# Kernel tuning notes

Hardware: AMD Instinct MI355X
Metric: run time of the kernel (lower is better)

The kernel has to match this reference:

```python
import jax, jax.numpy as jnp
import numpy as np

B, S, H, NH = 2, 2048, 4096, 32
D = H // NH  # head_dim = 128


def setup_inputs() -> dict:
    key = jax.random.key(0)
    ks = jax.random.split(key, 9)
    s = 1.0 / np.sqrt(H)
    return {
        "hidden_state": jax.random.normal(ks[0], (B, S, H), jnp.float32),
        "Wq": jax.random.normal(ks[1], (H, H), jnp.float32) * s,
        "bq": jax.random.normal(ks[2], (H,), jnp.float32) * 0.01,
        "Wk": jax.random.normal(ks[3], (D, H), jnp.float32) * s,
        "bk": jax.random.normal(ks[4], (D,), jnp.float32) * 0.01,
        "Wv": jax.random.normal(ks[5], (D, H), jnp.float32) * s,
        "bv": jax.random.normal(ks[6], (D,), jnp.float32) * 0.01,
        "Wo": jax.random.normal(ks[7], (H, H), jnp.float32) * s,
        "bo": jax.random.normal(ks[8], (H,), jnp.float32) * 0.01,
    }


def reference(hidden_state, Wq, bq, Wk, bk, Wv, bv, Wo, bo):
    b = hidden_state.shape[0]
    # Projections (torch Linear: x @ W.T + b)
    q = hidden_state @ Wq.T + bq              # (b, s, H)
    k = hidden_state @ Wk.T + bk              # (b, s, D) single shared KV head
    v = hidden_state @ Wv.T + bv              # (b, s, D)
    q = q.reshape(b, -1, NH, D).transpose(0, 2, 1, 3)  # (b, nh, s, d)
    # scores: broadcast the single K head across all query heads
    scale = 1.0 / jnp.sqrt(jnp.float32(D))
    scores = jnp.einsum("bhqd,bkd->bhqk", q, k) * scale   # (b, nh, s, s)
    probs = jax.nn.softmax(scores, axis=-1)
    out = jnp.einsum("bhqk,bkd->bhqd", probs, v)           # (b, nh, s, d)
    # Faithful to source: transpose(-1,-2) then view(b, -1, nh*d)
    out = jnp.swapaxes(out, -1, -2).reshape(b, -1, NH * D)  # (b, s, H) scrambled layout
    return out @ Wo.T + bo
```

## Files before the change

### kernel.cpp

```cpp
#include <hip/hip_runtime.h>
#include <hip/hip_bf16.h>

typedef __attribute__((ext_vector_type(8))) short bf16x8;
typedef __attribute__((ext_vector_type(4))) float f32x4;
typedef __attribute__((ext_vector_type(4))) unsigned int u32x4;
typedef __attribute__((ext_vector_type(2))) unsigned int u32x2;

__device__ __forceinline__ unsigned short f2bf(float f) {
    unsigned u = __builtin_bit_cast(unsigned, f);
    u += 0x7FFFu + ((u >> 16) & 1u);
    return (unsigned short)(u >> 16);
}

__device__ __forceinline__ void async16(const void* g, void* l) {
    __builtin_amdgcn_global_load_lds(
        (const __attribute__((address_space(1))) unsigned int*)g,
        (__attribute__((address_space(3))) unsigned int*)l, 16, 0, 0);
}

template <int N> __device__ __forceinline__ void waitv() {
    if constexpr (N == 8)      asm volatile("s_waitcnt vmcnt(8)" ::: "memory");
    else if constexpr (N == 6) asm volatile("s_waitcnt vmcnt(6)" ::: "memory");
    else if constexpr (N == 4) asm volatile("s_waitcnt vmcnt(4)" ::: "memory");
    else if constexpr (N == 3) asm volatile("s_waitcnt vmcnt(3)" ::: "memory");
    else                       asm volatile("s_waitcnt vmcnt(0)" ::: "memory");
}
#define BARF() do { __builtin_amdgcn_s_barrier(); asm volatile("" ::: "memory"); } while (0)

__device__ __forceinline__ void pl32(unsigned &a, unsigned &b) {
    u32x2 r = __builtin_amdgcn_permlane32_swap(a, b, false, false);
    a = r[0]; b = r[1];
}
__device__ __forceinline__ void pl16(unsigned &a, unsigned &b) {
    u32x2 r = __builtin_amdgcn_permlane16_swap(a, b, false, false);
    a = r[0]; b = r[1];
}

__global__ void cvt_f32_bf16(const float* __restrict__ x, unsigned short* __restrict__ y, int n4) {
    const int stride = gridDim.x * blockDim.x;
    for (int i = blockIdx.x * blockDim.x + threadIdx.x; i < n4; i += stride) {
        const float4 v = ((const float4*)x)[i];
        ushort4 o;
        o.x = f2bf(v.x); o.y = f2bf(v.y); o.z = f2bf(v.z); o.w = f2bf(v.w);
        ((ushort4*)y)[i] = o;
    }
}

template <int MREP, int MODE>
__global__ __launch_bounds__(512, 2) void gemm256(
    const unsigned short* __restrict__ A, const unsigned short* __restrict__ Bt,
    const float* __restrict__ b0, const float* __restrict__ b1, const float* __restrict__ b2,
    void* __restrict__ o0, unsigned short* __restrict__ o1, unsigned short* __restrict__ o2)
{
    constexpr int K = 4096, NT = 128;
    constexpr int ACALLS = MREP / 4;
    constexpr int CALLS  = ACALLS + 2;
    constexpr int ASH    = MREP * 1024;
    constexpr int SLOT   = ASH + 8192;
    __shared__ __align__(16) unsigned short lds[4 * SLOT];

    const int tid  = threadIdx.x;
    const int w    = tid >> 6, lane = tid & 63;
    const int l16  = lane & 15, quad = lane >> 4;
    const int wm   = w >> 2, wn = w & 3;

    int bx, by;
    {
        const int wg = (int)blockIdx.x;
        if constexpr (MODE == 1) {
            const int wgp = (wg & 7) * 68 + (wg >> 3);
            bx = wgp / 32; by = wgp % 32;
        } else {
            const int wgp = (wg & 7) * 32 + (wg >> 3);
            bx = wgp / 16; by = wgp % 16;
        }
    }
    const int m0 = by * (MREP * 32);
    const int n0 = bx * 256;

    const int srow = lane >> 2;
    const int schk = ((lane & 3) ^ ((lane >> 3) & 3)) * 8;
    const unsigned short* gAs[ACALLS];
#pragma unroll
    for (int c = 0; c < ACALLS; ++c)
        gAs[c] = A + (size_t)(m0 + (w * ACALLS + c) * 16 + srow) * K + schk;
    const unsigned short* gBs[2];
#pragma unroll
    for (int c = 0; c < 2; ++c)
        gBs[c] = Bt + (size_t)(n0 + (w * 2 + c) * 16 + srow) * K + schk;

    const int swz8 = (quad ^ ((l16 >> 1) & 3)) * 8;
    const int aoff = (wm * (MREP * 16) + l16) * 32 + swz8;
    const int boff = ASH + (wn * 64 + l16) * 32 + swz8;

    f32x4 acc[MREP][4] = {};

#define STAGE(tt) do { \
    unsigned short* lb = &lds[((tt) & 3) * SLOT]; \
    _Pragma("unroll") \
    for (int c = 0; c < ACALLS; ++c) \
        async16(gAs[c] + (tt) * 32, lb + (w * ACALLS + c) * 512); \
    _Pragma("unroll") \
    for (int c = 0; c < 2; ++c) \
        async16(gBs[c] + (tt) * 32, lb + ASH + (w * 2 + c) * 512); \
} while (0)

#define BODY(tt) do { \
    const unsigned short* lb = &lds[((tt) & 3) * SLOT]; \
    bf16x8 af[MREP], bfr[4]; \
    _Pragma("unroll") \
    for (int i = 0; i < MREP; ++i) af[i] = *(const bf16x8*)(lb + aoff + i * 512); \
    _Pragma("unroll") \
    for (int j = 0; j < 4; ++j)    bfr[j] = *(const bf16x8*)(lb + boff + j * 512); \
    __builtin_amdgcn_s_setprio(1); \
    _Pragma("unroll") \
    for (int i = 0; i < MREP; ++i) { \
        _Pragma("unroll") \
        for (int j = 0; j < 4; ++j) \
            acc[i][j] = __builtin_amdgcn_mfma_f32_16x16x32_bf16(af[i], bfr[j], acc[i][j], 0, 0, 0); \
    } \
    __builtin_amdgcn_s_setprio(0); \
} while (0)

    STAGE(0); STAGE(1); STAGE(2);
    for (int t = 0; t < NT - 3; ++t) {
        waitv<CALLS * 2>();
        BARF();
        STAGE(t + 3);
        BODY(t);
    }
    waitv<CALLS * 2>(); BARF(); BODY(NT - 3);
    waitv<CALLS>();     BARF(); BODY(NT - 2);
    waitv<0>();         BARF(); BODY(NT - 1);

#undef STAGE
#undef BODY

    if constexpr (MODE == 0) {
        float* C = (float*)o0;
#pragma unroll
        for (int j = 0; j < 4; ++j) {
            const int n = n0 + wn * 64 + j * 16 + l16;
            const float bb = b0[n];
#pragma unroll
            for (int i = 0; i < MREP; ++i) {
                const int mb = m0 + wm * (MREP * 16) + i * 16 + quad * 4;
#pragma unroll
                for (int r = 0; r < 4; ++r)
                    C[(size_t)(mb + r) * 4096 + n] = acc[i][j][r] + bb;
            }
        }
    } else {
        unsigned short* q_out = (unsigned short*)o0;
        const int nw0 = n0 + wn * 64;
        if (nw0 < 4096) {
#pragma unroll
            for (int j = 0; j < 4; ++j) {
                const int n = nw0 + j * 16 + l16;
                const float bb = b0[n];
#pragma unroll
                for (int i = 0; i < MREP; ++i) {
                    const int mb = m0 + wm * (MREP * 16) + i * 16 + quad * 4;
#pragma unroll
                    for (int r = 0; r < 4; ++r)
                        q_out[(size_t)(mb + r) * 4096 + n] = f2bf(acc[i][j][r] + bb);
                }
            }
        } else if (nw0 < 4224) {
#pragma unroll
            for (int j = 0; j < 4; ++j) {
                const int d = nw0 - 4096 + j * 16 + l16;
                const float bb = b1[d];
#pragma unroll
                for (int i = 0; i < MREP; ++i) {
                    const int mb = m0 + wm * (MREP * 16) + i * 16 + quad * 4;
#pragma unroll
                    for (int r = 0; r < 4; ++r)
                        o1[(size_t)(mb + r) * 128 + d] = f2bf(acc[i][j][r] + bb);
                }
            }
        } else {
#pragma unroll
            for (int j = 0; j < 4; ++j) {
                const int d = nw0 - 4224 + j * 16 + l16;
                const float bb = b2[d];
#pragma unroll
                for (int i = 0; i < MREP; ++i) {
                    const int mb = m0 + wm * (MREP * 16) + i * 16 + quad * 4;
                    ushort4 o;
                    o.x = f2bf(acc[i][j][0] + bb);
                    o.y = f2bf(acc[i][j][1] + bb);
                    o.z = f2bf(acc[i][j][2] + bb);
                    o.w = f2bf(acc[i][j][3] + bb);
                    *(ushort4*)(o2 + (size_t)((mb >> 11) * 128 + d) * 2048 + (mb & 2047)) = o;
                }
            }
        }
    }
}

__global__ __launch_bounds__(256, 4) void attn_mqa(
    const unsigned short* __restrict__ Q,
    const unsigned short* __restrict__ Kb,
    const unsigned short* __restrict__ vT,
    unsigned short* __restrict__ scr)
{
    constexpr int S = 2048, D = 128, H = 4096;
    constexpr float CSC = 0.0883883476483184f * 1.4426950408889634f;

    __shared__ __align__(16) unsigned short lds[17536];

    const int tid = threadIdx.x;
    const int w = tid >> 6, lane = tid & 63;
    const int l16 = lane & 15, quad = lane >> 4;
    const int qb = blockIdx.x & 15;
    const int h  = (blockIdx.x >> 4) & 31;
    const int b  = blockIdx.x >> 9;
    const int q0 = qb * 128;

    bf16x8 qf[2][4];
#pragma unroll
    for (int mi = 0; mi < 2; ++mi)
#pragma unroll
        for (int ks = 0; ks < 4; ++ks)
            qf[mi][ks] = *(const bf16x8*)(Q + (size_t)(b * S + q0 + w * 32 + mi * 16 + l16) * H
                                            + h * D + ks * 32 + quad * 8);

    f32x4 Oa[2][8] = {};
    float l_run[2] = {};

    const unsigned short* gK = Kb + (size_t)(b * S + l16) * D + quad * 8;
    const unsigned short* gV = vT + (size_t)(b * 128 + l16) * 2048 + quad * 8;

#define ASTAGE(tt) do { \
    unsigned short* buf = &lds[((tt) & 1) * 8192]; \
    const int kv0s = (tt) * 32; \
    _Pragma("unroll") \
    for (int c2 = 0; c2 < 2; ++c2) { \
        const int c = w * 2 + c2; \
        async16(gK + (size_t)(kv0s + (c >> 2) * 16) * D + (c & 3) * 32, buf + c * 512); \
        async16(gV + (size_t)(c * 16) * 2048 + kv0s, buf + 4096 + c * 512); \
    } \
} while (0)

    ASTAGE(0);
    for (int t = 0; t < 64; ++t) {
        waitv<0>();
        BARF();
        if (t < 63) ASTAGE(t + 1);

        const unsigned short* Kl = &lds[(t & 1) * 8192];
        const unsigned short* Vl = Kl + 4096;

        f32x4 sf[2][2] = {};
#pragma unroll
        for (int ct = 0; ct < 2; ++ct)
#pragma unroll
            for (int ks = 0; ks < 4; ++ks) {
                const bf16x8 kf = *(const bf16x8*)&Kl[(ct * 4 + ks) * 512 + lane * 8];
#pragma unroll
                for (int mi = 0; mi < 2; ++mi)
                    sf[mi][ct] = __builtin_amdgcn_mfma_f32_16x16x32_bf16(kf, qf[mi][ks], sf[mi][ct], 0, 0, 0);
            }

        bf16x8 pa[2];
#pragma unroll
        for (int mi = 0; mi < 2; ++mi) {
            unsigned cw[2][2];
#pragma unroll
            for (int ct = 0; ct < 2; ++ct) {
                const float p0 = exp2f(sf[mi][ct][0] * CSC);
                const float p1 = exp2f(sf[mi][ct][1] * CSC);
                const float p2 = exp2f(sf[mi][ct][2] * CSC);
                const float p3 = exp2f(sf[mi][ct][3] * CSC);
                l_run[mi] += (p0 + p1) + (p2 + p3);
                asm("v_cvt_pk_bf16_f32 %0, %1, %2" : "=v"(cw[ct][0]) : "v"(p0), "v"(p1));
                asm("v_cvt_pk_bf16_f32 %0, %1, %2" : "=v"(cw[ct][1]) : "v"(p2), "v"(p3));
            }
            unsigned c0 = cw[0][0], c1 = cw[0][1];
            unsigned d0 = cw[1][0], d1 = cw[1][1];
            pl32(c0, d0); pl16(c0, d0);
            pl32(c1, d1); pl16(c1, d1);
            u32x4 t4; t4[0] = c0; t4[1] = c1; t4[2] = d0; t4[3] = d1;
            pa[mi] = __builtin_bit_cast(bf16x8, t4);
        }

        __builtin_amdgcn_s_setprio(1);
#pragma unroll
        for (int nt = 0; nt < 8; ++nt) {
            const bf16x8 vf = *(const bf16x8*)&Vl[nt * 512 + lane * 8];
#pragma unroll
            for (int mi = 0; mi < 2; ++mi)
                Oa[mi][nt] = __builtin_amdgcn_mfma_f32_16x16x32_bf16(pa[mi], vf, Oa[mi][nt], 0, 0, 0);
        }
        __builtin_amdgcn_s_setprio(0);
    }
#undef ASTAGE

    float iv[2][4];
#pragma unroll
    for (int mi = 0; mi < 2; ++mi) {
        float l = l_run[mi];
        l += __shfl_xor(l, 16);
        l += __shfl_xor(l, 32);
        const float linv = 1.f / l;
#pragma unroll
        for (int i = 0; i < 4; ++i)
            iv[mi][i] = __shfl(linv, quad * 4 + i);
    }

    __syncthreads();
#pragma unroll
    for (int mi = 0; mi < 2; ++mi)
#pragma unroll
        for (int nt = 0; nt < 8; ++nt)
#pragma unroll
            for (int i = 0; i < 4; ++i)
                lds[(nt * 16 + l16) * 136 + w * 32 + mi * 16 + quad * 4 + i] =
                    f2bf(Oa[mi][nt][i] * iv[mi][i]);
    __syncthreads();

    const int d = tid >> 1, qh = tid & 1;
    unsigned short* op = scr + (size_t)(b * S + h * 64 + (d >> 1)) * H + (d & 1) * 2048 + q0 + qh * 64;
#pragma unroll
    for (int j = 0; j < 8; ++j)
        *(int4*)(op + j * 8) = *(const int4*)&lds[d * 136 + qh * 64 + j * 8];
}

extern "C" void kernel_launch(void* const* d_in, const int* in_sizes, int n_in,
                              void* d_out, int out_size, void* d_ws, size_t ws_size,
                              hipStream_t stream) {
    (void)in_sizes; (void)n_in; (void)out_size; (void)ws_size;
    const float* hidden = (const float*)d_in[0];
    const float* Wq = (const float*)d_in[1];
    const float* bq = (const float*)d_in[2];
    const float* Wk = (const float*)d_in[3];
    const float* bk = (const float*)d_in[4];
    const float* Wv = (const float*)d_in[5];
    const float* bv = (const float*)d_in[6];
    const float* Wo = (const float*)d_in[7];
    const float* bo = (const float*)d_in[8];

    char* ws = (char*)d_ws;
    const size_t MB = 1048576;
    unsigned short* hb   = (unsigned short*)(ws);
    unsigned short* scr  = hb;
    unsigned short* Wcat = (unsigned short*)(ws + 32 * MB);
    unsigned short* Wob  = Wcat;
    unsigned short* q_b  = (unsigned short*)(ws + 68 * MB);
    unsigned short* k_b  = (unsigned short*)(ws + 100 * MB);
    unsigned short* vT   = (unsigned short*)(ws + 101 * MB);

    cvt_f32_bf16<<<1024, 256, 0, stream>>>(hidden, hb, 16777216 / 4);
    cvt_f32_bf16<<<1024, 256, 0, stream>>>(Wq, Wcat, 16777216 / 4);
    cvt_f32_bf16<<<256, 256, 0, stream>>>(Wk, Wcat + 16777216, 524288 / 4);
    cvt_f32_bf16<<<256, 256, 0, stream>>>(Wv, Wcat + 17301504, 524288 / 4);

    gemm256<4, 1><<<dim3(544), 512, 0, stream>>>(hb, Wcat, bq, bk, bv,
                                                 (void*)q_b, k_b, vT);
    cvt_f32_bf16<<<1024, 256, 0, stream>>>(Wo, Wob, 16777216 / 4);
    attn_mqa<<<1024, 256, 0, stream>>>(q_b, k_b, vT, scr);
    gemm256<8, 0><<<dim3(256), 512, 0, stream>>>(scr, Wob, bo, nullptr, nullptr,
                                                 (void*)d_out, nullptr, nullptr);
}
```

Baseline: 725.1 us.

## Fuse input conversions, triple-buffer GEMM for occupancy, fold softmax scale into Q

Merges the four f32-to-bf16 conversion launches into one kernel. The GEMM drops from a 4-slot to a 3-slot LDS ring with rotating offsets and raises launch bounds to 4 blocks per CU. The output projection moves to the smaller MREP=4 tile with 512 blocks and a new block mapping. The softmax scale and log2e factor are folded into the Q projection epilogue, removing a multiply per score. Attention writes its output in two halves so it needs less LDS, with launch bounds raised to 5. Together these aim to cut launch overhead and raise occupancy, at the cost of a shallower prefetch pipeline and Q values that are rounded to bf16 after scaling.

```diff
diff --git a/kernel.cpp b/kernel.cpp
--- a/kernel.cpp
+++ b/kernel.cpp
@@ -46,8 +46,29 @@
     }
 }
 
+__global__ void cvt4_f32_bf16(
+    const float* __restrict__ h, const float* __restrict__ wq,
+    const float* __restrict__ wk, const float* __restrict__ wv,
+    unsigned short* __restrict__ hb, unsigned short* __restrict__ wcat)
+{
+    constexpr int NH = 4194304, NW = 4194304, NK = 131072;
+    constexpr int TOT = NH + NW + NK + NK;
+    const int stride = gridDim.x * blockDim.x;
+    for (int i = blockIdx.x * blockDim.x + threadIdx.x; i < TOT; i += stride) {
+        const float* src; unsigned short* dst; int j;
+        if (i < NH)            { src = h;  dst = hb;              j = i; }
+        else if (i < NH + NW)  { src = wq; dst = wcat;            j = i - NH; }
+        else if (i < NH + NW + NK) { src = wk; dst = wcat + 16777216; j = i - NH - NW; }
+        else                   { src = wv; dst = wcat + 17301504; j = i - NH - NW - NK; }
+        const float4 v = ((const float4*)src)[j];
+        ushort4 o;
+        o.x = f2bf(v.x); o.y = f2bf(v.y); o.z = f2bf(v.z); o.w = f2bf(v.w);
+        ((ushort4*)dst)[j] = o;
+    }
+}
+
 template <int MREP, int MODE>
-__global__ __launch_bounds__(512, 2) void gemm256(
+__global__ __launch_bounds__(512, 4) void gemm256(
     const unsigned short* __restrict__ A, const unsigned short* __restrict__ Bt,
     const float* __restrict__ b0, const float* __restrict__ b1, const float* __restrict__ b2,
     void* __restrict__ o0, unsigned short* __restrict__ o1, unsigned short* __restrict__ o2)
@@ -57,7 +78,7 @@
     constexpr int CALLS  = ACALLS + 2;
     constexpr int ASH    = MREP * 1024;
     constexpr int SLOT   = ASH + 8192;
-    __shared__ __align__(16) unsigned short lds[4 * SLOT];
+    __shared__ __align__(16) unsigned short lds[3 * SLOT];
 
     const int tid  = threadIdx.x;
     const int w    = tid >> 6, lane = tid & 63;
@@ -71,8 +92,8 @@
             const int wgp = (wg & 7) * 68 + (wg >> 3);
             bx = wgp / 32; by = wgp % 32;
         } else {
-            const int wgp = (wg & 7) * 32 + (wg >> 3);
-            bx = wgp / 16; by = wgp % 16;
+            const int wgp = (wg & 7) * 64 + (wg >> 3);
+            bx = wgp / 32; by = wgp % 32;
         }
     }
     const int m0 = by * (MREP * 32);
@@ -95,8 +116,8 @@
 
     f32x4 acc[MREP][4] = {};
 
-#define STAGE(tt) do { \
-    unsigned short* lb = &lds[((tt) & 3) * SLOT]; \
+#define STAGE(OB, tt) do { \
+    unsigned short* lb = &lds[(OB)]; \
     _Pragma("unroll") \
     for (int c = 0; c < ACALLS; ++c) \
         async16(gAs[c] + (tt) * 32, lb + (w * ACALLS + c) * 512); \
@@ -105,8 +126,8 @@
         async16(gBs[c] + (tt) * 32, lb + ASH + (w * 2 + c) * 512); \
 } while (0)
 
-#define BODY(tt) do { \
-    const unsigned short* lb = &lds[((tt) & 3) * SLOT]; \
+#define BODY(OB) do { \
+    const unsigned short* lb = &lds[(OB)]; \
     bf16x8 af[MREP], bfr[4]; \
     _Pragma("unroll") \
     for (int i = 0; i < MREP; ++i) af[i] = *(const bf16x8*)(lb + aoff + i * 512); \
@@ -122,16 +143,17 @@
     __builtin_amdgcn_s_setprio(0); \
 } while (0)
 
-    STAGE(0); STAGE(1); STAGE(2);
-    for (int t = 0; t < NT - 3; ++t) {
-        waitv<CALLS * 2>();
+    STAGE(0, 0); STAGE(SLOT, 1);
+    int oa = 0, ob = SLOT, oc = 2 * SLOT;
+    for (int t = 0; t < NT - 2; ++t) {
+        waitv<CALLS>();
         BARF();
-        STAGE(t + 3);
-        BODY(t);
-    }
-    waitv<CALLS * 2>(); BARF(); BODY(NT - 3);
-    waitv<CALLS>();     BARF(); BODY(NT - 2);
-    waitv<0>();         BARF(); BODY(NT - 1);
+        STAGE(oc, t + 2);
+        BODY(oa);
+        const int tmp = oa; oa = ob; ob = oc; oc = tmp;
+    }
+    waitv<CALLS>(); BARF(); BODY(oa);
+    waitv<0>();     BARF(); BODY(ob);
 
 #undef STAGE
 #undef BODY
@@ -151,6 +173,7 @@
             }
         }
     } else {
+        constexpr float CSC = 0.0883883476483184f * 1.4426950408889634f;
         unsigned short* q_out = (unsigned short*)o0;
         const int nw0 = n0 + wn * 64;
         if (nw0 < 4096) {
@@ -163,7 +186,7 @@
                     const int mb = m0 + wm * (MREP * 16) + i * 16 + quad * 4;
 #pragma unroll
                     for (int r = 0; r < 4; ++r)
-                        q_out[(size_t)(mb + r) * 4096 + n] = f2bf(acc[i][j][r] + bb);
+                        q_out[(size_t)(mb + r) * 4096 + n] = f2bf((acc[i][j][r] + bb) * CSC);
                 }
             }
         } else if (nw0 < 4224) {
@@ -199,16 +222,15 @@
     }
 }
 
-__global__ __launch_bounds__(256, 4) void attn_mqa(
+__global__ __launch_bounds__(256, 5) void attn_mqa(
     const unsigned short* __restrict__ Q,
     const unsigned short* __restrict__ Kb,
     const unsigned short* __restrict__ vT,
     unsigned short* __restrict__ scr)
 {
     constexpr int S = 2048, D = 128, H = 4096;
-    constexpr float CSC = 0.0883883476483184f * 1.4426950408889634f;
-
-    __shared__ __align__(16) unsigned short lds[17536];
+
+    __shared__ __align__(16) unsigned short lds[16384];
 
     const int tid = threadIdx.x;
     const int w = tid >> 6, lane = tid & 63;
@@ -269,10 +291,10 @@
             unsigned cw[2][2];
 #pragma unroll
             for (int ct = 0; ct < 2; ++ct) {
-                const float p0 = exp2f(sf[mi][ct][0] * CSC);
-                const float p1 = exp2f(sf[mi][ct][1] * CSC);
-                const float p2 = exp2f(sf[mi][ct][2] * CSC);
-                const float p3 = exp2f(sf[mi][ct][3] * CSC);
+                const float p0 = exp2f(sf[mi][ct][0]);
+                const float p1 = exp2f(sf[mi][ct][1]);
+                const float p2 = exp2f(sf[mi][ct][2]);
+                const float p3 = exp2f(sf[mi][ct][3]);
                 l_run[mi] += (p0 + p1) + (p2 + p3);
                 asm("v_cvt_pk_bf16_f32 %0, %1, %2" : "=v"(cw[ct][0]) : "v"(p0), "v"(p1));
                 asm("v_cvt_pk_bf16_f32 %0, %1, %2" : "=v"(cw[ct][1]) : "v"(p2), "v"(p3));
@@ -309,22 +331,25 @@
             iv[mi][i] = __shfl(linv, quad * 4 + i);
     }
 
-    __syncthreads();
-#pragma unroll
-    for (int mi = 0; mi < 2; ++mi)
-#pragma unroll
-        for (int nt = 0; nt < 8; ++nt)
-#pragma unroll
-            for (int i = 0; i < 4; ++i)
-                lds[(nt * 16 + l16) * 136 + w * 32 + mi * 16 + quad * 4 + i] =
-                    f2bf(Oa[mi][nt][i] * iv[mi][i]);
-    __syncthreads();
-
-    const int d = tid >> 1, qh = tid & 1;
-    unsigned short* op = scr + (size_t)(b * S + h * 64 + (d >> 1)) * H + (d & 1) * 2048 + q0 + qh * 64;
-#pragma unroll
-    for (int j = 0; j < 8; ++j)
-        *(int4*)(op + j * 8) = *(const int4*)&lds[d * 136 + qh * 64 + j * 8];
+#pragma unroll
+    for (int p = 0; p < 2; ++p) {
+        __syncthreads();
+#pragma unroll
+        for (int mi = 0; mi < 2; ++mi)
+#pragma unroll
+            for (int nt = 0; nt < 4; ++nt)
+#pragma unroll
+                for (int i = 0; i < 4; ++i)
+                    lds[(nt * 16 + l16) * 136 + w * 32 + mi * 16 + quad * 4 + i] =
+                        f2bf(Oa[mi][p * 4 + nt][i] * iv[mi][i]);
+        __syncthreads();
+        const int dl = tid >> 2, qq = tid & 3;
+        const int d = p * 64 + dl;
+        unsigned short* op = scr + (size_t)(b * S + h * 64 + (d >> 1)) * H + (d & 1) * 2048 + q0 + qq * 32;
+#pragma unroll
+        for (int j = 0; j < 4; ++j)
+            *(int4*)(op + j * 8) = *(const int4*)&lds[dl * 136 + qq * 32 + j * 8];
+    }
 }
 
 extern "C" void kernel_launch(void* const* d_in, const int* in_sizes, int n_in,
@@ -351,15 +376,12 @@
     unsigned short* k_b  = (unsigned short*)(ws + 100 * MB);
     unsigned short* vT   = (unsigned short*)(ws + 101 * MB);
 
-    cvt_f32_bf16<<<1024, 256, 0, stream>>>(hidden, hb, 16777216 / 4);
-    cvt_f32_bf16<<<1024, 256, 0, stream>>>(Wq, Wcat, 16777216 / 4);
-    cvt_f32_bf16<<<256, 256, 0, stream>>>(Wk, Wcat + 16777216, 524288 / 4);
-    cvt_f32_bf16<<<256, 256, 0, stream>>>(Wv, Wcat + 17301504, 524288 / 4);
+    cvt4_f32_bf16<<<2048, 256, 0, stream>>>(hidden, Wq, Wk, Wv, hb, Wcat);
 
     gemm256<4, 1><<<dim3(544), 512, 0, stream>>>(hb, Wcat, bq, bk, bv,
                                                  (void*)q_b, k_b, vT);
     cvt_f32_bf16<<<1024, 256, 0, stream>>>(Wo, Wob, 16777216 / 4);
     attn_mqa<<<1024, 256, 0, stream>>>(q_b, k_b, vT, scr);
-    gemm256<8, 0><<<dim3(256), 512, 0, stream>>>(scr, Wob, bo, nullptr, nullptr,
+    gemm256<4, 0><<<dim3(512), 512, 0, stream>>>(scr, Wob, bo, nullptr, nullptr,
                                                  (void*)d_out, nullptr, nullptr);
 }
```

Measured after the change: 1.349 ms. 86.1% more time.
